# Performance work log

Hardware: AMD Instinct MI355X
Metric: run time of the kernel (lower is better)

The kernel has to match this reference:

```python
import jax, jax.numpy as jnp
import numpy as np

S = 384    # size2d (s = 128*3)
D1 = 3     # lattice dimension+1 (hardcoded d=d1=3 in the module)

# canonical simplex offsets built exactly as in __init__:
# start [[0,1,2]]*3, then canonical[-1:,1]=-2, canonical[-2:,2]=-1
CANONICAL = jnp.array([[0, 1, 2],
                       [0, 1, -1],
                       [0, -2, -1]], dtype=jnp.int32)


def setup_inputs() -> dict:
    key = jax.random.key(0)
    k1, k2, k3 = jax.random.split(key, 3)
    B, N = 64, 8192
    # get_model passes x[:, :3] * (s // 2); emulate unit-cube points scaled by 192
    pc1 = (jax.random.uniform(k1, (B, 3, N), jnp.float32) * 2.0 - 1.0) * (S // 2)
    features = jax.random.normal(k2, (B, 3, N), jnp.float32)
    tm = jax.random.normal(k3, (B, 3, 3), jnp.float32)
    # F.normalize(trans_matrix, dim=1)
    trans_mat = tm / jnp.maximum(jnp.linalg.norm(tm, axis=1, keepdims=True), 1e-12)
    return {"pc1": pc1, "features": features, "trans_mat": trans_mat}


def reference(pc1, features, trans_mat):
    B, _, N = pc1.shape
    # ---- get_keys_and_barycentric ----
    elevated = jnp.einsum('bij,bjn->bin', trans_mat, pc1)          # [B,3,N]
    greedy = jnp.round(elevated / D1) * D1
    el_minus_gr = elevated - greedy
    # rank = inverse permutation of descending argsort along lattice axis
    idx = jnp.argsort(-el_minus_gr, axis=1)
    rank = jnp.argsort(idx, axis=1).astype(jnp.int32)              # [B,3,N]
    remainder_sum = jnp.sum(greedy, axis=1, keepdims=True) / D1    # [B,1,N] (exact ints)
    rank_f = rank.astype(jnp.float32)
    cond = ((rank_f >= D1 - remainder_sum) & (remainder_sum > 0)) | \
           ((rank_f < -remainder_sum) & (remainder_sum < 0))
    sign = jnp.where(remainder_sum > 0, -1.0, 0.0) + jnp.where(remainder_sum < 0, 1.0, 0.0)
    shift = D1 * sign * cond.astype(jnp.float32)                   # [B,3,N]
    greedy = greedy + shift
    rank = rank + shift.astype(jnp.int32) + remainder_sum.astype(jnp.int32)
    greedy_i = greedy.astype(jnp.int32)
    # NOTE: in the torch source the two non-accumulating index-assigns
    # (barycentric[b, 3-rank, n] += E then barycentric[b, 3-rank, n] -= E,
    # with self.d == self.d1 == 3) write to identical index sets and cancel
    # exactly; after the final `+= 1.0 + barycentric[:, d1]` the barycentric
    # weights are 1 on lattice channel 0 and 0 elsewhere. Reproduce faithfully.
    barycentric = jnp.zeros((B, D1, N), pc1.dtype).at[:, 0, :].set(1.0)
    keys = greedy_i[:, :, :, None] + CANONICAL[rank]               # [B,3,N,3]

    # ---- splat into dense 2D grid ----
    coord = keys[:, :2].reshape(B, 2, D1 * N)                      # [B,2,3N]
    offset = coord.min(axis=2)                                     # [B,2]
    coord = coord - offset[:, :, None]
    tmp = barycentric[:, None, :, :] * features[:, :, None, :]     # [B,3feat,3lat,N]
    tmp = jnp.transpose(tmp, (0, 1, 3, 2)).reshape(B, 3, D1 * N)   # [B,3,3N]
    tmp = jnp.transpose(tmp, (0, 2, 1))                            # [B,3N,3]
    pts_pick = (-offset) % D1                                      # [B,2]
    oob = coord >= S                                               # [B,2,3N]
    coord = jnp.where(oob, 0, coord)
    tmp = jnp.where(oob.any(axis=1)[:, :, None], 0.0, tmp)
    bidx = jnp.arange(B)[:, None]
    # sparse_coo.to_dense() accumulates duplicate coords -> scatter-add
    splatted = jnp.zeros((B, S, S, 3), pc1.dtype).at[bidx, coord[:, 0], coord[:, 1]].add(tmp)
    # filter_2d[i] = splatted[i, pp0::3, pp1::3][:S//3, :S//3]
    base = jnp.arange(S // D1) * D1                                # [128]
    rows = pts_pick[:, 0:1] + base[None, :]                        # [B,128]
    cols = pts_pick[:, 1:2] + base[None, :]
    filt = jax.vmap(lambda sp, r, c: sp[r][:, c])(splatted, rows, cols)  # [B,128,128,3]
    return filt
```

## Files before the change

### kernel.cpp

```cpp
#include <hip/hip_runtime.h>
#include <math.h>

#define NB     64
#define NPTS   8192
#define S2D    384
#define GW     128
#define QROWS  32
#define BLK    1024
#define PPT    (NPTS / BLK)
#define ACCN   (QROWS * GW * 3)

__global__ __launch_bounds__(1024) void fused_splat(const float* __restrict__ pc1,
                                                    const float* __restrict__ feat,
                                                    const float* __restrict__ tm,
                                                    float* __restrict__ out) {
    const int b   = blockIdx.x >> 2;
    const int q   = blockIdx.x & 3;
    const int tid = threadIdx.x;

    __shared__ __align__(16) float acc[ACCN];
    __shared__ int s_off[2];

    if (tid < 2) s_off[tid] = 0x7FFFFFFF;
#pragma unroll
    for (int i = 0; i < ACCN / BLK; i++)
        acc[tid + i * BLK] = 0.0f;

    float t[9];
#pragma unroll
    for (int i = 0; i < 9; i++) t[i] = tm[b * 9 + i];

    int gi0[PPT], gi1[PPT];
    int m0 = 0x7FFFFFFF, m1 = 0x7FFFFFFF;

#pragma unroll
    for (int k = 0; k < PPT; k++) {
        const int n = tid + k * BLK;
        const float p0 = pc1[((size_t)b * 3 + 0) * NPTS + n];
        const float p1 = pc1[((size_t)b * 3 + 1) * NPTS + n];
        const float p2 = pc1[((size_t)b * 3 + 2) * NPTS + n];

        float g[3], v[3];
#pragma unroll
        for (int i = 0; i < 3; i++) {
            float e  = fmaf(t[i*3+2], p2, fmaf(t[i*3+1], p1, t[i*3+0] * p0));
            float qq = __fdiv_rn(e, 3.0f);
            g[i] = rintf(qq) * 3.0f;
            v[i] = e - g[i];
        }

        int rank[3];
#pragma unroll
        for (int i = 0; i < 3; i++) {
            int r = 0;
#pragma unroll
            for (int j = 0; j < 3; j++)
                if (v[j] > v[i] || (v[j] == v[i] && j < i)) r++;
            rank[i] = r;
        }

        const float rs_f = __fdiv_rn(g[0] + g[1] + g[2], 3.0f);
        const int   rs   = (int)rs_f;

        int gi[2];
#pragma unroll
        for (int i = 0; i < 2; i++) {
            const float rank_f = (float)rank[i];
            const bool cond = ((rank_f >= 3.0f - rs_f) && (rs_f > 0.0f)) ||
                              ((rank_f <  -rs_f)       && (rs_f < 0.0f));
            const float sign  = (rs_f > 0.0f ? -1.0f : 0.0f) + (rs_f < 0.0f ? 1.0f : 0.0f);
            const float shift = 3.0f * sign * (cond ? 1.0f : 0.0f);
            gi[i] = (int)(g[i] + shift);
            const int rfin = rank[i] + (int)shift + rs;
            const int cl = min(max(rfin, 0), 2);
            const int cand = gi[i] - cl;
            if (i == 0) m0 = min(m0, cand); else m1 = min(m1, cand);
        }
        gi0[k] = gi[0];
        gi1[k] = gi[1];
    }

#pragma unroll
    for (int off = 32; off > 0; off >>= 1) {
        m0 = min(m0, __shfl_down(m0, off));
        m1 = min(m1, __shfl_down(m1, off));
    }
    if ((tid & 63) == 0) {
        atomicMin(&s_off[0], m0);
        atomicMin(&s_off[1], m1);
    }
    __syncthreads();

    const int off0 = s_off[0], off1 = s_off[1];
    const int pp0 = ((-off0) % 3 + 3) % 3;
    const int pp1 = ((-off1) % 3 + 3) % 3;
    const int rlo = q * QROWS, rhi = rlo + QROWS;

#pragma unroll
    for (int k = 0; k < PPT; k++) {
        const int n  = tid + k * BLK;
        const int c0 = gi0[k] - off0;
        const int c1 = gi1[k] - off1;
        if (c0 < S2D && c1 < S2D) {
            const int i0 = (c0 - pp0) / 3;
            if (i0 >= rlo && i0 < rhi) {
                const int j0 = (c1 - pp1) / 3;
                float* dst = acc + (((i0 - rlo) * GW) + j0) * 3;
                atomicAdd(dst + 0, feat[((size_t)b * 3 + 0) * NPTS + n]);
                atomicAdd(dst + 1, feat[((size_t)b * 3 + 1) * NPTS + n]);
                atomicAdd(dst + 2, feat[((size_t)b * 3 + 2) * NPTS + n]);
            }
        }
    }
    __syncthreads();

    float4* __restrict__ dst4 = (float4*)(out + ((size_t)b * GW + rlo) * GW * 3);
    const float4* __restrict__ src4 = (const float4*)acc;
#pragma unroll
    for (int i = 0; i < ACCN / (4 * BLK); i++)
        dst4[tid + i * BLK] = src4[tid + i * BLK];
}

extern "C" void kernel_launch(void* const* d_in, const int* in_sizes, int n_in,
                              void* d_out, int out_size, void* d_ws, size_t ws_size,
                              hipStream_t stream) {
    const float* pc1  = (const float*)d_in[0];
    const float* feat = (const float*)d_in[1];
    const float* tm   = (const float*)d_in[2];
    float* out = (float*)d_out;

    fused_splat<<<NB * 4, BLK, 0, stream>>>(pc1, feat, tm, out);
}
```

Measured before the change: 94.30 us.

## Split lattice key computation from splatting into two kernels via workspace

The single fused kernel made all four row-quarter blocks of a batch recompute lattice keys for all 8192 points. The work is now split in two. A first kernel computes each point's packed lattice key once, with each block handling a quarter of the points, and writes per-block minimum offsets to the workspace. A second kernel reads those keys, reduces the partial minima and scatters features into the shared-memory accumulator. The math moves to integers, and a block-to-XCD mapping groups each batch's blocks on one XCD for cache locality. The cost is an extra launch and a global round-trip of 2 MB of keys.

```diff
diff --git a/kernel.cpp b/kernel.cpp
--- a/kernel.cpp
+++ b/kernel.cpp
@@ -7,77 +7,68 @@
 #define GW     128
 #define QROWS  32
 #define BLK    1024
-#define PPT    (NPTS / BLK)
 #define ACCN   (QROWS * GW * 3)
 
-__global__ __launch_bounds__(1024) void fused_splat(const float* __restrict__ pc1,
-                                                    const float* __restrict__ feat,
-                                                    const float* __restrict__ tm,
-                                                    float* __restrict__ out) {
-    const int b   = blockIdx.x >> 2;
-    const int q   = blockIdx.x & 3;
-    const int tid = threadIdx.x;
+#define WS_KEYS_OFF 1024
 
-    __shared__ __align__(16) float acc[ACCN];
-    __shared__ int s_off[2];
+__global__ __launch_bounds__(1024) void lattice_keys(const float* __restrict__ pc1,
+                                                     const float* __restrict__ tm,
+                                                     unsigned int* __restrict__ ws) {
+    const int x    = blockIdx.x;
+    const int xcd  = x & 7;
+    const int slot = x >> 3;
+    const int b    = xcd * 8 + (slot >> 2);
+    const int part = slot & 3;
+    const int tid  = threadIdx.x;
 
-    if (tid < 2) s_off[tid] = 0x7FFFFFFF;
-#pragma unroll
-    for (int i = 0; i < ACCN / BLK; i++)
-        acc[tid + i * BLK] = 0.0f;
+    __shared__ int s_min[2];
+    if (tid < 2) s_min[tid] = 0x7FFFFFFF;
+    __syncthreads();
 
     float t[9];
 #pragma unroll
     for (int i = 0; i < 9; i++) t[i] = tm[b * 9 + i];
 
-    int gi0[PPT], gi1[PPT];
     int m0 = 0x7FFFFFFF, m1 = 0x7FFFFFFF;
 
 #pragma unroll
-    for (int k = 0; k < PPT; k++) {
-        const int n = tid + k * BLK;
+    for (int k = 0; k < 2; k++) {
+        const int n = part * 2048 + tid + k * BLK;
         const float p0 = pc1[((size_t)b * 3 + 0) * NPTS + n];
         const float p1 = pc1[((size_t)b * 3 + 1) * NPTS + n];
         const float p2 = pc1[((size_t)b * 3 + 2) * NPTS + n];
 
-        float g[3], v[3];
+        float v[3];
+        int   ur[3];
 #pragma unroll
         for (int i = 0; i < 3; i++) {
             float e  = fmaf(t[i*3+2], p2, fmaf(t[i*3+1], p1, t[i*3+0] * p0));
             float qq = __fdiv_rn(e, 3.0f);
-            g[i] = rintf(qq) * 3.0f;
-            v[i] = e - g[i];
+            float rq = rintf(qq);
+            ur[i] = (int)rq;
+            v[i]  = e - rq * 3.0f;
         }
 
-        int rank[3];
+        const int rs = ur[0] + ur[1] + ur[2];
+
+        unsigned int key = 0;
 #pragma unroll
-        for (int i = 0; i < 3; i++) {
+        for (int i = 0; i < 2; i++) {
             int r = 0;
 #pragma unroll
             for (int j = 0; j < 3; j++)
                 if (v[j] > v[i] || (v[j] == v[i] && j < i)) r++;
-            rank[i] = r;
+            const bool cond = ((r >= 3 - rs) && (rs > 0)) ||
+                              ((r <  -rs)   && (rs < 0));
+            const int s    = cond ? (rs > 0 ? -1 : 1) : 0;
+            const int u    = ur[i] + s;
+            const int rfin = r + 3 * s + rs;
+            const int cl   = min(max(rfin, 0), 2);
+            const int cand = 3 * u - cl;
+            if (i == 0) { m0 = min(m0, cand); key |= (unsigned)(u + 512); }
+            else        { m1 = min(m1, cand); key |= ((unsigned)(u + 512)) << 16; }
         }
-
-        const float rs_f = __fdiv_rn(g[0] + g[1] + g[2], 3.0f);
-        const int   rs   = (int)rs_f;
-
-        int gi[2];
-#pragma unroll
-        for (int i = 0; i < 2; i++) {
-            const float rank_f = (float)rank[i];
-            const bool cond = ((rank_f >= 3.0f - rs_f) && (rs_f > 0.0f)) ||
-                              ((rank_f <  -rs_f)       && (rs_f < 0.0f));
-            const float sign  = (rs_f > 0.0f ? -1.0f : 0.0f) + (rs_f < 0.0f ? 1.0f : 0.0f);
-            const float shift = 3.0f * sign * (cond ? 1.0f : 0.0f);
-            gi[i] = (int)(g[i] + shift);
-            const int rfin = rank[i] + (int)shift + rs;
-            const int cl = min(max(rfin, 0), 2);
-            const int cand = gi[i] - cl;
-            if (i == 0) m0 = min(m0, cand); else m1 = min(m1, cand);
-        }
-        gi0[k] = gi[0];
-        gi1[k] = gi[1];
+        ws[WS_KEYS_OFF + (size_t)b * NPTS + n] = key;
     }
 
 #pragma unroll
@@ -86,30 +77,58 @@
         m1 = min(m1, __shfl_down(m1, off));
     }
     if ((tid & 63) == 0) {
-        atomicMin(&s_off[0], m0);
-        atomicMin(&s_off[1], m1);
+        atomicMin(&s_min[0], m0);
+        atomicMin(&s_min[1], m1);
     }
     __syncthreads();
+    if (tid == 0) {
+        ws[b * 8 + part * 2 + 0] = (unsigned int)s_min[0];
+        ws[b * 8 + part * 2 + 1] = (unsigned int)s_min[1];
+    }
+}
 
-    const int off0 = s_off[0], off1 = s_off[1];
-    const int pp0 = ((-off0) % 3 + 3) % 3;
-    const int pp1 = ((-off1) % 3 + 3) % 3;
-    const int rlo = q * QROWS, rhi = rlo + QROWS;
+__global__ __launch_bounds__(1024) void splat_out(const float* __restrict__ feat,
+                                                  const unsigned int* __restrict__ ws,
+                                                  float* __restrict__ out) {
+    const int x    = blockIdx.x;
+    const int xcd  = x & 7;
+    const int slot = x >> 3;
+    const int b    = xcd * 8 + (slot >> 2);
+    const int q    = slot & 3;
+    const int tid  = threadIdx.x;
+
+    __shared__ __align__(16) float acc[ACCN];
+    __shared__ int s_part[8];
+
+    if (tid < 8) s_part[tid] = ((const int*)ws)[b * 8 + tid];
+#pragma unroll
+    for (int i = 0; i < ACCN / BLK; i++)
+        acc[tid + i * BLK] = 0.0f;
+    __syncthreads();
+
+    const int off0 = min(min(s_part[0], s_part[2]), min(s_part[4], s_part[6]));
+    const int off1 = min(min(s_part[1], s_part[3]), min(s_part[5], s_part[7]));
+    const int pp0  = ((-off0) % 3 + 3) % 3;
+    const int pp1  = ((-off1) % 3 + 3) % 3;
+    const int U0   = (off0 + pp0) / 3;
+    const int U1   = (off1 + pp1) / 3;
+    const int rlo  = q * QROWS;
+
+    const unsigned int* __restrict__ keys = ws + WS_KEYS_OFF + (size_t)b * NPTS;
+    const float* __restrict__ fb = feat + (size_t)b * 3 * NPTS;
 
 #pragma unroll
-    for (int k = 0; k < PPT; k++) {
-        const int n  = tid + k * BLK;
-        const int c0 = gi0[k] - off0;
-        const int c1 = gi1[k] - off1;
-        if (c0 < S2D && c1 < S2D) {
-            const int i0 = (c0 - pp0) / 3;
-            if (i0 >= rlo && i0 < rhi) {
-                const int j0 = (c1 - pp1) / 3;
-                float* dst = acc + (((i0 - rlo) * GW) + j0) * 3;
-                atomicAdd(dst + 0, feat[((size_t)b * 3 + 0) * NPTS + n]);
-                atomicAdd(dst + 1, feat[((size_t)b * 3 + 1) * NPTS + n]);
-                atomicAdd(dst + 2, feat[((size_t)b * 3 + 2) * NPTS + n]);
-            }
+    for (int k = 0; k < NPTS / BLK; k++) {
+        const int n = tid + k * BLK;
+        const unsigned int key = keys[n];
+        const int i0 = (int)(key & 0xFFFFu) - 512 - U0;
+        const int j0 = (int)(key >> 16)     - 512 - U1;
+        const unsigned int ri = (unsigned int)(i0 - rlo);
+        if (ri < QROWS && (unsigned int)j0 < GW) {
+            float* dst = acc + (ri * GW + (unsigned int)j0) * 3;
+            atomicAdd(dst + 0, fb[n]);
+            atomicAdd(dst + 1, fb[NPTS + n]);
+            atomicAdd(dst + 2, fb[2 * NPTS + n]);
         }
     }
     __syncthreads();
@@ -128,6 +147,8 @@
     const float* feat = (const float*)d_in[1];
     const float* tm   = (const float*)d_in[2];
     float* out = (float*)d_out;
+    unsigned int* ws  = (unsigned int*)d_ws;
 
-    fused_splat<<<NB * 4, BLK, 0, stream>>>(pc1, feat, tm, out);
+    lattice_keys<<<NB * 4, BLK, 0, stream>>>(pc1, tm, ws);
+    splat_out<<<NB * 4, BLK, 0, stream>>>(feat, ws, out);
 }
```

Result: no change. 92.93 us, median of 2 (-1.5%).
